# Performance work log

Hardware: AMD Instinct MI355X
Metric: run time of the kernel (lower is better)

The kernel has to match this reference:

```python
import jax, jax.numpy as jnp
import numpy as np
from jax import lax

# norse LIFParameters defaults: tau_syn_inv=200, tau_mem_inv=100, v_leak=0,
# v_th=1, v_reset=0, dt=0.001; alpha=0.5 (super-spike surrogate slope).
DT = 1e-3
TAU_SYN_INV = 200.0
TAU_MEM_INV = 100.0
V_LEAK = 0.0
V_TH = 1.0
V_RESET = 0.0
ALPHA = 0.5
NUM_STEPS = 100


@jax.custom_vjp
def heaviside_super(x):
    # forward: hard threshold; backward: SuperSpike surrogate (norse.threshold)
    return (x > 0).astype(x.dtype)

def _hs_fwd(x):
    return heaviside_super(x), x

def _hs_bwd(x, g):
    return (g / (ALPHA * jnp.abs(x) + 1.0) ** 2,)

heaviside_super.defvjp(_hs_fwd, _hs_bwd)


def lif_step(cur, v, i):
    # norse lif_step: Euler update of membrane v and synaptic current i
    v_dec = v + DT * TAU_MEM_INV * ((V_LEAK - v) + i)
    i_dec = i * (1.0 - DT * TAU_SYN_INV)
    z = heaviside_super(v_dec - V_TH)
    v_new = (1.0 - z) * v_dec + z * V_RESET
    i_new = i_dec + cur
    return z, v_new, i_new


def conv2d(x, w, b):
    y = lax.conv_general_dilated(x, w, window_strides=(1, 1), padding='VALID',
                                 dimension_numbers=('NCHW', 'OIHW', 'NCHW'))
    return y + b[None, :, None, None]


def maxpool2(x):
    return lax.reduce_window(x, -jnp.inf, lax.max, (1, 1, 2, 2), (1, 1, 2, 2), 'VALID')


def snn_forward(x, w1, b1, w2, b2, wf, bf):
    B = x.shape[0]
    # conv1(x) is identical every timestep in the torch code; hoist it.
    cur1 = maxpool2(conv2d(x, w1, b1))  # [B,13,6,6]
    v1 = jnp.zeros_like(cur1); i1 = jnp.zeros_like(cur1)
    v2 = jnp.zeros((B, w2.shape[0], 3, 3), x.dtype); i2 = jnp.zeros_like(v2)
    v3 = jnp.zeros((B, wf.shape[0]), x.dtype); i3 = jnp.zeros_like(v3)

    def step(carry, _):
        v1, i1, v2, i2, v3, i3 = carry
        spk1, v1, i1 = lif_step(cur1, v1, i1)          # [B,13,6,6]
        cur2 = conv2d(spk1, w2, b2)                    # [B,64,3,3]
        spk2, v2, i2 = lif_step(cur2, v2, i2)
        cur3 = spk2.reshape(B, -1) @ wf.T + bf         # [B,2]
        spk3, v3, i3 = lif_step(cur3, v3, i3)
        return (v1, i1, v2, i2, v3, i3), (spk3, v3)

    _, (spk3_seq, v3_seq) = lax.scan(step, (v1, i1, v2, i2, v3, i3), None, length=NUM_STEPS)
    spk_out = spk3_seq.sum(0)   # sum of output spikes over time, [B,2]
    return spk_out, v3_seq      # v3_seq = stacked mem3_record, [T,B,2]


def setup_inputs() -> dict:
    key = jax.random.key(0)
    ks = jax.random.split(key, 7)
    B = 2048
    x = jax.random.normal(ks[0], (B, 1, 16, 16), jnp.float32)
    w1 = jax.random.normal(ks[1], (13, 1, 4, 4), jnp.float32) * 0.25
    b1 = jax.random.normal(ks[2], (13,), jnp.float32) * 0.1
    w2 = jax.random.normal(ks[3], (64, 13, 4, 4), jnp.float32) * (1.0 / np.sqrt(13 * 16))
    b2 = jax.random.normal(ks[4], (64,), jnp.float32) * 0.05
    wf = jax.random.normal(ks[5], (2, 576), jnp.float32) * (1.0 / np.sqrt(576))
    bf = jax.random.normal(ks[6], (2,), jnp.float32) * 0.05
    return {"x": x, "w1": w1, "b1": b1, "w2": w2, "b2": b2, "wf": wf, "bf": bf}


def reference(x, w1, b1, w2, b2, wf, bf):
    return snn_forward(x, w1, b1, w2, b2, wf, bf)
```

## Files before the change

### kernel.cpp

```cpp
#include <hip/hip_runtime.h>


#define NSTEPS 100
#define NCHUNK 50
#define IMSTRIDE 272
#define ZIMG (48 * IMSTRIDE)
#define Z2S 612
#define Z2T (4 * Z2S)
#define Z2PAR (2 * Z2T)

typedef __attribute__((ext_vector_type(4))) int i32x4;

__device__ __forceinline__ void conv1_row(const float* __restrict__ xs,
                                          const float* __restrict__ w1s,
                                          float b1v, int y, float* cur) {
    float cr[2][12];
    #pragma unroll
    for (int rr = 0; rr < 2; ++rr) {
        const int cy = 2 * y + rr;
        #pragma unroll
        for (int cx = 0; cx < 12; ++cx) {
            float a = 0.f;
            #pragma unroll
            for (int ky = 0; ky < 4; ++ky)
            #pragma unroll
            for (int kx = 0; kx < 4; ++kx)
                a = fmaf(xs[(cy + ky) * 16 + cx + kx], w1s[ky * 4 + kx], a);
            cr[rr][cx] = a + b1v;
        }
    }
    #pragma unroll
    for (int px = 0; px < 6; ++px)
        cur[px] = fmaxf(fmaxf(cr[0][2 * px], cr[0][2 * px + 1]),
                        fmaxf(cr[1][2 * px], cr[1][2 * px + 1]));
}

__device__ __forceinline__ void lif1_row(float* v1, float* i1, const float* cur,
                                         unsigned char* pb, int ic, int y) {
    unsigned zb[6];
    #pragma unroll
    for (int xx = 0; xx < 6; ++xx) {
        const float vd = v1[xx] + 0.1f * (i1[xx] - v1[xx]);
        i1[xx] = i1[xx] * 0.8f + cur[xx];
        const bool sp = vd > 1.0f;
        v1[xx] = sp ? 0.0f : vd;
        zb[xx] = sp ? 1u : 0u;
    }
    const unsigned q0 = zb[0] | (zb[1] << 8) | (zb[2] << 16) | (zb[3] << 24);
    const unsigned q1 = zb[1] | (zb[2] << 8) | (zb[3] << 16) | (zb[4] << 24);
    const unsigned q2 = zb[2] | (zb[3] << 8) | (zb[4] << 16) | (zb[5] << 24);
    #pragma unroll
    for (int ky = 0; ky < 4; ++ky) {
        const int py = y - ky;
        if (0 <= py && py <= 2) {
            unsigned char* b = pb - ky * (3 * IMSTRIDE) + 4 * ((ky + ic) & 3);
            *(unsigned*)(b)                = q0;
            *(unsigned*)(b + IMSTRIDE)     = q1;
            *(unsigned*)(b + 2 * IMSTRIDE) = q2;
        }
    }
}

__global__ __launch_bounds__(256, 2)
void snn_kernel(const float* __restrict__ x,
                const float* __restrict__ w1,
                const float* __restrict__ b1,
                const float* __restrict__ w2,
                const float* __restrict__ b2,
                const float* __restrict__ wf,
                const float* __restrict__ bf,
                float* __restrict__ out, int B)
{
    __shared__ __align__(16) unsigned char s_im[4 * ZIMG];
    __shared__ __align__(16) unsigned short s_z2h[2 * Z2PAR];
    __shared__ __align__(16) float s_x[4 * 256];
    __shared__ __align__(16) float s_w1[13 * 16];
    __shared__ float s_b1[13];

    const int tid  = threadIdx.x;
    const int wave = tid >> 6, lane = tid & 63;
    const int quad = lane >> 4, col = lane & 15;

    ((float4*)(s_x + wave * 256))[lane] =
        ((const float4*)(x + (size_t)(blockIdx.x * 4 + wave) * 256))[lane];
    if (tid < 208) s_w1[tid] = w1[tid];
    if (tid < 13)  s_b1[tid] = b1[tid];
    for (int i = tid; i < 4 * ZIMG / 16; i += 256)
        ((uint4*)s_im)[i] = make_uint4(0, 0, 0, 0);
    __syncthreads();

    int sA, icA, yA, sB = 0, icB = 0, yB = 0;
    { const int R = tid;       sA = R / 78; int r = R - 78 * sA; icA = r / 6; yA = r - 6 * icA; }
    if (tid < 56) { const int R = tid + 256; sB = R / 78; int r = R - 78 * sB; icB = r / 6; yB = r - 6 * icB; }

    float cur1a[6], v1a[6], i1a[6], cur1b[6], v1b[6], i1b[6];
    conv1_row(s_x + sA * 256, s_w1 + icA * 16, s_b1[icA], yA, cur1a);
    if (tid < 56) conv1_row(s_x + sB * 256, s_w1 + icB * 16, s_b1[icB], yB, cur1b);
    #pragma unroll
    for (int j = 0; j < 6; ++j) { v1a[j] = i1a[j] = 0.f; v1b[j] = i1b[j] = 0.f; }

    const int pbOffA = (9 * sA + 3 * yA) * IMSTRIDE + 16 * icA;
    const int pbOffB = (9 * sB + 3 * yB) * IMSTRIDE + 16 * icB;

    i32x4 A1[4], A2[4], A3[4];
    float Mrow;
    {
        const float* wrow = w2 + (size_t)(wave * 16 + col) * 208;
        float M = 1e-20f;
        for (int k = 0; k < 208; ++k) M = fmaxf(M, fabsf(wrow[k]));
        Mrow = M;
        const float inv = 127.0f / M;
        const float q1s = M * (1.0f / 127.0f);
        const float q2s = M * (1.0f / (127.0f * 127.0f));
        #pragma unroll
        for (int kt = 0; kt < 4; ++kt) {
            i32x4 w1v = {0, 0, 0, 0}, w2v = {0, 0, 0, 0}, w3v = {0, 0, 0, 0};
            #pragma unroll
            for (int j = 0; j < 16; ++j) {
                const int kp = kt * 64 + quad * 16 + j;
                const int W = kp >> 2, kx = kp & 3;
                const int ic = W >> 2, ky = ((W & 3) - ic) & 3;
                const float w = (ic < 13) ? wrow[ic * 16 + ky * 4 + kx] : 0.f;
                const float b1f = rintf(w * inv);
                const float r1  = fmaf(b1f, -q1s, w);
                const float b2f = rintf(r1 * inv * 127.0f);
                const float r2  = fmaf(b2f, -q2s, r1);
                const float b3f = rintf(r2 * inv * 127.0f * 127.0f);
                const int wi = j >> 2, sh = (j & 3) * 8;
                w1v[wi] |= ((int)b1f & 0xFF) << sh;
                w2v[wi] |= ((int)b2f & 0xFF) << sh;
                w3v[wi] |= ((int)b3f & 0xFF) << sh;
            }
            A1[kt] = w1v; A2[kt] = w2v; A3[kt] = w3v;
        }
    }
    float sc1[4], sc2[4], sc3[4];
    #pragma unroll
    for (int r = 0; r < 4; ++r) {
        const float Mr = __shfl(Mrow, quad * 4 + r);
        sc1[r] = Mr * (1.0f / 127.0f);
        sc2[r] = Mr * (1.0f / (127.0f * 127.0f));
        sc3[r] = Mr * (1.0f / (127.0f * 127.0f * 127.0f));
    }

    float wf0[9], wf1[9];
    #pragma unroll
    for (int q = 0; q < 9; ++q) {
        wf0[q] = wf[lane * 9 + q];
        wf1[q] = wf[576 + lane * 9 + q];
    }
    const float bfv0 = bf[0], bfv1 = bf[1];
    float b2r[4];
    #pragma unroll
    for (int r = 0; r < 4; ++r) b2r[r] = b2[wave * 16 + quad * 4 + r];

    int bpo[3];
    int zwo[3];
    bool zv[3];
    #pragma unroll
    for (int nt = 0; nt < 3; ++nt) {
        const int n = nt * 16 + col;
        bpo[nt] = n * IMSTRIDE + quad * 16;
        zv[nt] = (n < 36);
        const int slz = n / 9, pos = n - slz * 9;
        zwo[nt] = slz * Z2S + pos * 68 + wave * 16 + quad * 4;
    }

    float v2[12], i2[12];
    #pragma unroll
    for (int p = 0; p < 12; ++p) { v2[p] = 0.f; i2[p] = 0.f; }
    float v3a = 0.f, i3a = 0.f, v3b = 0.f, i3b = 0.f, sum0 = 0.f, sum1 = 0.f;

    const int sG = blockIdx.x * 4 + wave;
    float* outv = out + (size_t)2 * B;

    auto fc_step = [&](const unsigned short* zs, int tp) {
        float p0 = 0.f, p1 = 0.f;
        #pragma unroll
        for (int q = 0; q < 9; ++q) {
            const float z = __uint_as_float(((unsigned)zs[q * 68 + lane]) << 16);
            p0 = fmaf(z, wf0[q], p0);
            p1 = fmaf(z, wf1[q], p1);
        }
        #pragma unroll
        for (int off = 32; off > 0; off >>= 1) {
            p0 += __shfl_xor(p0, off);
            p1 += __shfl_xor(p1, off);
        }
        const float c3a = p0 + bfv0, c3b = p1 + bfv1;
        const float vd0 = v3a + 0.1f * (i3a - v3a);
        const float vd1 = v3b + 0.1f * (i3b - v3b);
        i3a = i3a * 0.8f + c3a;
        i3b = i3b * 0.8f + c3b;
        const bool q0 = vd0 > 1.0f, q1 = vd1 > 1.0f;
        v3a = q0 ? 0.0f : vd0;
        v3b = q1 ? 0.0f : vd1;
        sum0 += q0 ? 1.0f : 0.0f;
        sum1 += q1 ? 1.0f : 0.0f;
        if (lane == 0)
            *(float2*)(outv + (size_t)tp * 2 * B + 2 * sG) = make_float2(v3a, v3b);
    };

    auto chunk = [&](int ch, int P) {
        unsigned char* zb0 = s_im + (2 * P) * ZIMG;
        unsigned char* zb1 = s_im + (2 * P + 1) * ZIMG;
        lif1_row(v1a, i1a, cur1a, zb0 + pbOffA, icA, yA);
        if (tid < 56) lif1_row(v1b, i1b, cur1b, zb0 + pbOffB, icB, yB);
        lif1_row(v1a, i1a, cur1a, zb1 + pbOffA, icA, yA);
        if (tid < 56) lif1_row(v1b, i1b, cur1b, zb1 + pbOffB, icB, yB);
        __syncthreads();

        if (ch) {
            const unsigned short* zp = s_z2h + (P ^ 1) * Z2PAR + wave * Z2S;
            fc_step(zp, 2 * ch - 2);
            fc_step(zp + Z2T, 2 * ch - 1);
        }

        #pragma unroll
        for (int tl = 0; tl < 2; ++tl) {
            const unsigned char* zbuf = s_im + (2 * P + tl) * ZIMG;
            i32x4 c1a = {0,0,0,0}, c1b = c1a, c1c = c1a;
            i32x4 c2a = c1a, c2b = c1a, c2c = c1a;
            i32x4 c3a_ = c1a, c3b_ = c1a, c3c = c1a;
            #pragma unroll
            for (int kt = 0; kt < 4; ++kt) {
                const i32x4 B0 = *(const i32x4*)(zbuf + bpo[0] + kt * 64);
                const i32x4 B1 = *(const i32x4*)(zbuf + bpo[1] + kt * 64);
                const i32x4 B2v = *(const i32x4*)(zbuf + bpo[2] + kt * 64);
                c1a = __builtin_amdgcn_mfma_i32_16x16x64_i8(A1[kt], B0,  c1a, 0, 0, 0);
                c1b = __builtin_amdgcn_mfma_i32_16x16x64_i8(A1[kt], B1,  c1b, 0, 0, 0);
                c1c = __builtin_amdgcn_mfma_i32_16x16x64_i8(A1[kt], B2v, c1c, 0, 0, 0);
                c2a = __builtin_amdgcn_mfma_i32_16x16x64_i8(A2[kt], B0,  c2a, 0, 0, 0);
                c2b = __builtin_amdgcn_mfma_i32_16x16x64_i8(A2[kt], B1,  c2b, 0, 0, 0);
                c2c = __builtin_amdgcn_mfma_i32_16x16x64_i8(A2[kt], B2v, c2c, 0, 0, 0);
                c3a_ = __builtin_amdgcn_mfma_i32_16x16x64_i8(A3[kt], B0,  c3a_, 0, 0, 0);
                c3b_ = __builtin_amdgcn_mfma_i32_16x16x64_i8(A3[kt], B1,  c3b_, 0, 0, 0);
                c3c = __builtin_amdgcn_mfma_i32_16x16x64_i8(A3[kt], B2v, c3c, 0, 0, 0);
            }

            const i32x4 L1[3] = {c1a, c1b, c1c};
            const i32x4 L2[3] = {c2a, c2b, c2c};
            const i32x4 L3[3] = {c3a_, c3b_, c3c};
            unsigned short* z2b = s_z2h + P * Z2PAR + tl * Z2T;
            #pragma unroll
            for (int nt = 0; nt < 3; ++nt) {
                unsigned zbits[4];
                #pragma unroll
                for (int r = 0; r < 4; ++r) {
                    const int p = nt * 4 + r;
                    const float cur2 =
                        fmaf(sc1[r], (float)L1[nt][r],
                        fmaf(sc2[r], (float)L2[nt][r],
                        fmaf(sc3[r], (float)L3[nt][r], b2r[r])));
                    const float vd = v2[p] + 0.1f * (i2[p] - v2[p]);
                    i2[p] = i2[p] * 0.8f + cur2;
                    const bool sp = vd > 1.0f;
                    v2[p] = sp ? 0.0f : vd;
                    zbits[r] = sp ? 0x3F80u : 0u;
                }
                if (zv[nt]) {
                    const unsigned lo = zbits[0] | (zbits[1] << 16);
                    const unsigned hi = zbits[2] | (zbits[3] << 16);
                    *(uint2*)(z2b + zwo[nt]) = make_uint2(lo, hi);
                }
            }
        }
    };

    #pragma unroll 1
    for (int cc = 0; cc < NCHUNK; cc += 2) {
        chunk(cc, 0);
        chunk(cc + 1, 1);
    }

    __syncthreads();
    {
        const unsigned short* zp = s_z2h + 1 * Z2PAR + wave * Z2S;
        fc_step(zp, NSTEPS - 2);
        fc_step(zp + Z2T, NSTEPS - 1);
    }

    if (lane == 0)
        *(float2*)(out + (size_t)2 * sG) = make_float2(sum0, sum1);
}

extern "C" void kernel_launch(void* const* d_in, const int* in_sizes, int n_in,
                              void* d_out, int out_size, void* d_ws, size_t ws_size,
                              hipStream_t stream)
{
    const float* x  = (const float*)d_in[0];
    const float* w1 = (const float*)d_in[1];
    const float* b1 = (const float*)d_in[2];
    const float* w2 = (const float*)d_in[3];
    const float* b2 = (const float*)d_in[4];
    const float* wf = (const float*)d_in[5];
    const float* bf = (const float*)d_in[6];
    float* out = (float*)d_out;

    const int B = in_sizes[0] / 256;
    const int grid = B / 4;

    hipLaunchKernelGGL(snn_kernel, dim3(grid), dim3(256), 0, stream,
                       x, w1, b1, w2, b2, wf, bf, out, B);
}
```

Measured before the change: 270.5 us.

## Pipeline per-timestep LIF1, conv2 MFMA and FC stages with single barrier per step

Replaces the two-timestep chunk schedule with a per-timestep software pipeline. Each step loads the spike tile into registers, runs the FC step for the previous timestep, issues the conv2 MFMAs, and then computes the layer-1 LIF spikes two timesteps ahead into a 4-deep ring of image buffers. The z2 spike buffer shrinks to double buffering. The aim is to overlap the LIF1 VALU work and the FC reductions with MFMA latency, at the cost of one barrier per timestep instead of one per two timesteps.

```diff
diff --git a/kernel.cpp b/kernel.cpp
--- a/kernel.cpp
+++ b/kernel.cpp
@@ -2,12 +2,10 @@
 
 
 #define NSTEPS 100
-#define NCHUNK 50
 #define IMSTRIDE 272
 #define ZIMG (48 * IMSTRIDE)
 #define Z2S 612
 #define Z2T (4 * Z2S)
-#define Z2PAR (2 * Z2T)
 
 typedef __attribute__((ext_vector_type(4))) int i32x4;
 
@@ -72,7 +70,7 @@
                 float* __restrict__ out, int B)
 {
     __shared__ __align__(16) unsigned char s_im[4 * ZIMG];
-    __shared__ __align__(16) unsigned short s_z2h[2 * Z2PAR];
+    __shared__ __align__(16) unsigned short s_z2h[2 * Z2T];
     __shared__ __align__(16) float s_x[4 * 256];
     __shared__ __align__(16) float s_w1[13 * 16];
     __shared__ float s_b1[13];
@@ -201,84 +199,84 @@
             *(float2*)(outv + (size_t)tp * 2 * B + 2 * sG) = make_float2(v3a, v3b);
     };
 
-    auto chunk = [&](int ch, int P) {
-        unsigned char* zb0 = s_im + (2 * P) * ZIMG;
-        unsigned char* zb1 = s_im + (2 * P + 1) * ZIMG;
-        lif1_row(v1a, i1a, cur1a, zb0 + pbOffA, icA, yA);
-        if (tid < 56) lif1_row(v1b, i1b, cur1b, zb0 + pbOffB, icB, yB);
-        lif1_row(v1a, i1a, cur1a, zb1 + pbOffA, icA, yA);
-        if (tid < 56) lif1_row(v1b, i1b, cur1b, zb1 + pbOffB, icB, yB);
+    lif1_row(v1a, i1a, cur1a, s_im + pbOffA, icA, yA);
+    if (tid < 56) lif1_row(v1b, i1b, cur1b, s_im + pbOffB, icB, yB);
+    lif1_row(v1a, i1a, cur1a, s_im + ZIMG + pbOffA, icA, yA);
+    if (tid < 56) lif1_row(v1b, i1b, cur1b, s_im + ZIMG + pbOffB, icB, yB);
+    __syncthreads();
+
+    auto body = [&](int t, int p4) {
+        const unsigned char* zbuf = s_im + p4 * ZIMG;
+        i32x4 Bf0[4], Bf1[4], Bf2[4];
+        #pragma unroll
+        for (int kt = 0; kt < 4; ++kt) {
+            Bf0[kt] = *(const i32x4*)(zbuf + bpo[0] + kt * 64);
+            Bf1[kt] = *(const i32x4*)(zbuf + bpo[1] + kt * 64);
+            Bf2[kt] = *(const i32x4*)(zbuf + bpo[2] + kt * 64);
+        }
+
+        if (t) fc_step(s_z2h + ((p4 ^ 1) & 1) * Z2T + wave * Z2S, t - 1);
+
+        i32x4 c1a = {0,0,0,0}, c1b = c1a, c1c = c1a;
+        i32x4 c2a = c1a, c2b = c1a, c2c = c1a;
+        i32x4 c3a_ = c1a, c3b_ = c1a, c3c = c1a;
+        #pragma unroll
+        for (int kt = 0; kt < 4; ++kt) {
+            c1a  = __builtin_amdgcn_mfma_i32_16x16x64_i8(A1[kt], Bf0[kt], c1a, 0, 0, 0);
+            c1b  = __builtin_amdgcn_mfma_i32_16x16x64_i8(A1[kt], Bf1[kt], c1b, 0, 0, 0);
+            c1c  = __builtin_amdgcn_mfma_i32_16x16x64_i8(A1[kt], Bf2[kt], c1c, 0, 0, 0);
+            c2a  = __builtin_amdgcn_mfma_i32_16x16x64_i8(A2[kt], Bf0[kt], c2a, 0, 0, 0);
+            c2b  = __builtin_amdgcn_mfma_i32_16x16x64_i8(A2[kt], Bf1[kt], c2b, 0, 0, 0);
+            c2c  = __builtin_amdgcn_mfma_i32_16x16x64_i8(A2[kt], Bf2[kt], c2c, 0, 0, 0);
+            c3a_ = __builtin_amdgcn_mfma_i32_16x16x64_i8(A3[kt], Bf0[kt], c3a_, 0, 0, 0);
+            c3b_ = __builtin_amdgcn_mfma_i32_16x16x64_i8(A3[kt], Bf1[kt], c3b_, 0, 0, 0);
+            c3c  = __builtin_amdgcn_mfma_i32_16x16x64_i8(A3[kt], Bf2[kt], c3c, 0, 0, 0);
+        }
+
+        const i32x4 L1[3] = {c1a, c1b, c1c};
+        const i32x4 L2[3] = {c2a, c2b, c2c};
+        const i32x4 L3[3] = {c3a_, c3b_, c3c};
+        unsigned short* z2b = s_z2h + (p4 & 1) * Z2T;
+        #pragma unroll
+        for (int nt = 0; nt < 3; ++nt) {
+            unsigned zbits[4];
+            #pragma unroll
+            for (int r = 0; r < 4; ++r) {
+                const int p = nt * 4 + r;
+                const float cur2 =
+                    fmaf(sc1[r], (float)L1[nt][r],
+                    fmaf(sc2[r], (float)L2[nt][r],
+                    fmaf(sc3[r], (float)L3[nt][r], b2r[r])));
+                const float vd = v2[p] + 0.1f * (i2[p] - v2[p]);
+                i2[p] = i2[p] * 0.8f + cur2;
+                const bool sp = vd > 1.0f;
+                v2[p] = sp ? 0.0f : vd;
+                zbits[r] = sp ? 0x3F80u : 0u;
+            }
+            if (zv[nt]) {
+                const unsigned lo = zbits[0] | (zbits[1] << 16);
+                const unsigned hi = zbits[2] | (zbits[3] << 16);
+                *(uint2*)(z2b + zwo[nt]) = make_uint2(lo, hi);
+            }
+        }
+
+        if (t < NSTEPS - 2) {
+            unsigned char* nb = s_im + ((p4 + 2) & 3) * ZIMG;
+            lif1_row(v1a, i1a, cur1a, nb + pbOffA, icA, yA);
+            if (tid < 56) lif1_row(v1b, i1b, cur1b, nb + pbOffB, icB, yB);
+        }
         __syncthreads();
-
-        if (ch) {
-            const unsigned short* zp = s_z2h + (P ^ 1) * Z2PAR + wave * Z2S;
-            fc_step(zp, 2 * ch - 2);
-            fc_step(zp + Z2T, 2 * ch - 1);
-        }
-
-        #pragma unroll
-        for (int tl = 0; tl < 2; ++tl) {
-            const unsigned char* zbuf = s_im + (2 * P + tl) * ZIMG;
-            i32x4 c1a = {0,0,0,0}, c1b = c1a, c1c = c1a;
-            i32x4 c2a = c1a, c2b = c1a, c2c = c1a;
-            i32x4 c3a_ = c1a, c3b_ = c1a, c3c = c1a;
-            #pragma unroll
-            for (int kt = 0; kt < 4; ++kt) {
-                const i32x4 B0 = *(const i32x4*)(zbuf + bpo[0] + kt * 64);
-                const i32x4 B1 = *(const i32x4*)(zbuf + bpo[1] + kt * 64);
-                const i32x4 B2v = *(const i32x4*)(zbuf + bpo[2] + kt * 64);
-                c1a = __builtin_amdgcn_mfma_i32_16x16x64_i8(A1[kt], B0,  c1a, 0, 0, 0);
-                c1b = __builtin_amdgcn_mfma_i32_16x16x64_i8(A1[kt], B1,  c1b, 0, 0, 0);
-                c1c = __builtin_amdgcn_mfma_i32_16x16x64_i8(A1[kt], B2v, c1c, 0, 0, 0);
-                c2a = __builtin_amdgcn_mfma_i32_16x16x64_i8(A2[kt], B0,  c2a, 0, 0, 0);
-                c2b = __builtin_amdgcn_mfma_i32_16x16x64_i8(A2[kt], B1,  c2b, 0, 0, 0);
-                c2c = __builtin_amdgcn_mfma_i32_16x16x64_i8(A2[kt], B2v, c2c, 0, 0, 0);
-                c3a_ = __builtin_amdgcn_mfma_i32_16x16x64_i8(A3[kt], B0,  c3a_, 0, 0, 0);
-                c3b_ = __builtin_amdgcn_mfma_i32_16x16x64_i8(A3[kt], B1,  c3b_, 0, 0, 0);
-                c3c = __builtin_amdgcn_mfma_i32_16x16x64_i8(A3[kt], B2v, c3c, 0, 0, 0);
-            }
-
-            const i32x4 L1[3] = {c1a, c1b, c1c};
-            const i32x4 L2[3] = {c2a, c2b, c2c};
-            const i32x4 L3[3] = {c3a_, c3b_, c3c};
-            unsigned short* z2b = s_z2h + P * Z2PAR + tl * Z2T;
-            #pragma unroll
-            for (int nt = 0; nt < 3; ++nt) {
-                unsigned zbits[4];
-                #pragma unroll
-                for (int r = 0; r < 4; ++r) {
-                    const int p = nt * 4 + r;
-                    const float cur2 =
-                        fmaf(sc1[r], (float)L1[nt][r],
-                        fmaf(sc2[r], (float)L2[nt][r],
-                        fmaf(sc3[r], (float)L3[nt][r], b2r[r])));
-                    const float vd = v2[p] + 0.1f * (i2[p] - v2[p]);
-                    i2[p] = i2[p] * 0.8f + cur2;
-                    const bool sp = vd > 1.0f;
-                    v2[p] = sp ? 0.0f : vd;
-                    zbits[r] = sp ? 0x3F80u : 0u;
-                }
-                if (zv[nt]) {
-                    const unsigned lo = zbits[0] | (zbits[1] << 16);
-                    const unsigned hi = zbits[2] | (zbits[3] << 16);
-                    *(uint2*)(z2b + zwo[nt]) = make_uint2(lo, hi);
-                }
-            }
-        }
     };
 
     #pragma unroll 1
-    for (int cc = 0; cc < NCHUNK; cc += 2) {
-        chunk(cc, 0);
-        chunk(cc + 1, 1);
-    }
-
-    __syncthreads();
-    {
-        const unsigned short* zp = s_z2h + 1 * Z2PAR + wave * Z2S;
-        fc_step(zp, NSTEPS - 2);
-        fc_step(zp + Z2T, NSTEPS - 1);
-    }
+    for (int t = 0; t < NSTEPS; t += 4) {
+        body(t, 0);
+        body(t + 1, 1);
+        body(t + 2, 2);
+        body(t + 3, 3);
+    }
+
+    fc_step(s_z2h + 1 * Z2T + wave * Z2S, NSTEPS - 1);
 
     if (lane == 0)
         *(float2*)(out + (size_t)2 * sG) = make_float2(sum0, sum1);
```

Result: slower. 356.0 us (+31.6%).
